# Kernel optimization log

Measured on AMD Instinct MI355X. Metric: run time of the kernel, lower is better.

Reference implementation:

```python
import jax, jax.numpy as jnp
import numpy as np

N = 100000      # nodes
E = 3200000     # edges (avg degree 32)
D = 128         # in_channels
H = 128         # hidden_channels
L = 4           # num_layers
G = 1000        # graphs in batch
C = 10          # out_channels
BN_EPS = 1e-5


def _init(key, shape, fan_in):
    return jax.random.normal(key, shape, jnp.float32) * jnp.float32(1.0 / np.sqrt(fan_in))


def setup_inputs() -> dict:
    key = jax.random.key(0)
    ks = jax.random.split(key, 12)
    x = jax.random.normal(ks[0], (N, D), jnp.float32)
    edge_index = jax.random.randint(ks[1], (2, E), 0, N)
    batch = jnp.sort(jax.random.randint(ks[2], (N,), 0, G))
    # stacked per-layer GINConv MLP params (in==hidden so all layers share shapes)
    W1 = _init(ks[3], (L, D, 2 * H), D)
    b1 = jnp.zeros((L, 2 * H), jnp.float32)
    g1 = jnp.ones((L, 2 * H), jnp.float32)
    bt1 = jnp.zeros((L, 2 * H), jnp.float32)
    W2 = _init(ks[4], (L, 2 * H, H), 2 * H)
    b2 = jnp.zeros((L, H), jnp.float32)
    g2 = jnp.ones((L, H), jnp.float32)
    bt2 = jnp.zeros((L, H), jnp.float32)
    eps = jnp.zeros((L,), jnp.float32)  # train_eps=True, init 0
    # final graph-level MLP
    Wm1 = _init(ks[5], (H, H), H)
    bm1 = jnp.zeros((H,), jnp.float32)
    gm = jnp.ones((H,), jnp.float32)
    btm = jnp.zeros((H,), jnp.float32)
    Wm2 = _init(ks[6], (H, C), H)
    bm2 = jnp.zeros((C,), jnp.float32)
    return dict(x=x, edge_index=edge_index, batch=batch, eps=eps,
                W1=W1, b1=b1, g1=g1, bt1=bt1, W2=W2, b2=b2, g2=g2, bt2=bt2,
                Wm1=Wm1, bm1=bm1, gm=gm, btm=btm, Wm2=Wm2, bm2=bm2)


def batchnorm(z, g, b):
    # training-mode BN: batch statistics, biased variance (torch semantics)
    m = jnp.mean(z, axis=0)
    v = jnp.mean(jnp.square(z - m), axis=0)
    return (z - m) * (g * jax.lax.rsqrt(v + BN_EPS)) + b


def reference(x, edge_index, batch, eps, W1, b1, g1, bt1, W2, b2, g2, bt2,
              Wm1, bm1, gm, btm, Wm2, bm2):
    src, dst = edge_index[0], edge_index[1]
    h = x
    for l in range(L):
        # GINConv: (1+eps)*x_i + sum_{j in N(i)} x_j, then MLP
        agg = jax.ops.segment_sum(h[src], dst, num_segments=N)  # [N, d]
        z = (1.0 + eps[l]) * h + agg
        z = jax.nn.relu(batchnorm(z @ W1[l] + b1[l], g1[l], bt1[l]))
        h = z @ W2[l] + b2[l]
        # outer per-layer BatchNorm + relu
        h = jax.nn.relu(batchnorm(h, g2[l], bt2[l]))
    # global_add_pool over graphs
    ge = jax.ops.segment_sum(h, batch, num_segments=G)  # [G, H]
    o = jax.nn.relu(batchnorm(ge @ Wm1 + bm1, gm, btm))  # dropout = identity (eval)
    return o @ Wm2 + bm2  # [G, C]
```

## Files before the change

kernel.cpp:

```cpp
#include <hip/hip_runtime.h>

#define N_NODES 100000
#define N_EDGES 3200000
#define NGRAPH  1000
#define NOUT    10
#define BN_EPS  1e-5f
#define CAP     96

#define SUM1 0
#define SQ1  256
#define S1   512
#define SH1  768
#define SUM2 1024
#define SQ2  1152
#define S2   1280
#define SH2  1408
#define SUMG 1536
#define SQG  1664
#define SG   1792
#define SHG  1920

typedef short v8s __attribute__((ext_vector_type(8)));
typedef float v4f __attribute__((ext_vector_type(4)));

__device__ __forceinline__ unsigned short f2bf(float x) {
    unsigned u = __float_as_uint(x);
    u += 0x7FFFu + ((u >> 16) & 1u);
    return (unsigned short)(u >> 16);
}
__device__ __forceinline__ float bf2f(unsigned short h) {
    return __uint_as_float(((unsigned)h) << 16);
}


__global__ void k_zero_i(int* p, int n) {
    int i = blockIdx.x * 256 + threadIdx.x;
    if (i < n) p[i] = 0;
}

__global__ void k_fillb(const int* __restrict__ ei, int* __restrict__ cnt,
                        int* __restrict__ csr) {
    const int lo = blockIdx.x * 12500;
    const int base = blockIdx.y * 2048 + threadIdx.x;
#pragma unroll
    for (int i = 0; i < 8; ++i) {
        int e = base + i * 256;
        if (e < N_EDGES) {
            int d = ei[N_EDGES + e];
            if ((unsigned)(d - lo) < 12500u) {
                int slot = atomicAdd(&cnt[d], 1);
                if (slot < CAP) csr[d * CAP + slot] = ei[e];
            }
        }
    }
}


__global__ void k_cvt0(const float* __restrict__ x, unsigned short* __restrict__ hb) {
    int i = blockIdx.x * 256 + threadIdx.x;
    float4 v = ((const float4*)x)[i];
    ushort4 o;
    o.x = f2bf(v.x); o.y = f2bf(v.y); o.z = f2bf(v.z); o.w = f2bf(v.w);
    ((ushort4*)hb)[i] = o;
}


__global__ void k_bnapply(const unsigned short* __restrict__ hb,
                          unsigned short* __restrict__ yb,
                          const float* __restrict__ s, const float* __restrict__ sh) {
    int i = blockIdx.x * 256 + threadIdx.x;
    int c16 = i & 15;
    uint4 u = ((const uint4*)hb)[i];
    float4 sA = ((const float4*)s)[c16 * 2], sB = ((const float4*)s)[c16 * 2 + 1];
    float4 hA = ((const float4*)sh)[c16 * 2], hB = ((const float4*)sh)[c16 * 2 + 1];
    float y0 = fmaxf(fmaf(__uint_as_float(u.x << 16),        sA.x, hA.x), 0.f);
    float y1 = fmaxf(fmaf(__uint_as_float(u.x & 0xffff0000u), sA.y, hA.y), 0.f);
    float y2 = fmaxf(fmaf(__uint_as_float(u.y << 16),        sA.z, hA.z), 0.f);
    float y3 = fmaxf(fmaf(__uint_as_float(u.y & 0xffff0000u), sA.w, hA.w), 0.f);
    float y4 = fmaxf(fmaf(__uint_as_float(u.z << 16),        sB.x, hB.x), 0.f);
    float y5 = fmaxf(fmaf(__uint_as_float(u.z & 0xffff0000u), sB.y, hB.y), 0.f);
    float y6 = fmaxf(fmaf(__uint_as_float(u.w << 16),        sB.z, hB.z), 0.f);
    float y7 = fmaxf(fmaf(__uint_as_float(u.w & 0xffff0000u), sB.w, hB.w), 0.f);
    uint4 o;
    o.x = (unsigned)f2bf(y0) | ((unsigned)f2bf(y1) << 16);
    o.y = (unsigned)f2bf(y2) | ((unsigned)f2bf(y3) << 16);
    o.z = (unsigned)f2bf(y4) | ((unsigned)f2bf(y5) << 16);
    o.w = (unsigned)f2bf(y6) | ((unsigned)f2bf(y7) << 16);
    ((uint4*)yb)[i] = o;
}


__global__ void k_wsplit(const float* __restrict__ W1l, const float* __restrict__ W2l,
                         unsigned short* __restrict__ w1h, unsigned short* __restrict__ w1lo,
                         unsigned short* __restrict__ w2h, unsigned short* __restrict__ w2lo) {
    int idx = blockIdx.x * 256 + threadIdx.x;
    if (idx < 32768) {
        float v = W1l[idx];
        int k = idx >> 8, n = idx & 255;
        unsigned short h = f2bf(v);
        unsigned short l = f2bf(v - bf2f(h));
        int o = n * 128 + k;
        w1h[o] = h; w1lo[o] = l;
    } else {
        int i2 = idx - 32768;
        float v = W2l[i2];
        int k = i2 >> 7, n = i2 & 127;
        unsigned short h = f2bf(v);
        unsigned short l = f2bf(v - bf2f(h));
        int o = n * 256 + k;
        w2h[o] = h; w2lo[o] = l;
    }
}


__launch_bounds__(256)
__global__ void k_agg(const unsigned short* __restrict__ yb, unsigned short* __restrict__ zh,
                      unsigned short* __restrict__ zl, const int* __restrict__ cnt,
                      const int* __restrict__ csr, const float* __restrict__ eps, int l,
                      float* __restrict__ stats) {
    if (blockIdx.x == 0) {
        int t = threadIdx.x;
        stats[SUM1 + t] = 0.f;
        stats[SQ1 + t] = 0.f;
        if (t < 128) { stats[SUM2 + t] = 0.f; stats[SQ2 + t] = 0.f; }
    }
    const int tid = threadIdx.x;
    const int wid = tid >> 6, lane = tid & 63;
    const int q = lane >> 4, sl = lane & 15;
    const int node = blockIdx.x * 16 + wid * 4 + q;
    const uint4* y4 = (const uint4*)yb;
    const size_t selfo = (size_t)node * 16 + sl;

    float epv = 1.f + eps[l];
    uint4 su = y4[selfo];
    float acc[8];
    acc[0] = epv * __uint_as_float(su.x << 16);
    acc[1] = epv * __uint_as_float(su.x & 0xffff0000u);
    acc[2] = epv * __uint_as_float(su.y << 16);
    acc[3] = epv * __uint_as_float(su.y & 0xffff0000u);
    acc[4] = epv * __uint_as_float(su.z << 16);
    acc[5] = epv * __uint_as_float(su.z & 0xffff0000u);
    acc[6] = epv * __uint_as_float(su.w << 16);
    acc[7] = epv * __uint_as_float(su.w & 0xffff0000u);

    int d = min(cnt[node], CAP);
    const int* row = csr + node * CAP;
    int t = 0;
    for (; t + 3 < d; t += 4) {
        int4 jv = *(const int4*)(row + t);
        uint4 v0 = y4[(size_t)jv.x * 16 + sl];
        uint4 v1 = y4[(size_t)jv.y * 16 + sl];
        uint4 v2 = y4[(size_t)jv.z * 16 + sl];
        uint4 v3 = y4[(size_t)jv.w * 16 + sl];
        acc[0] += __uint_as_float(v0.x << 16);
        acc[1] += __uint_as_float(v0.x & 0xffff0000u);
        acc[2] += __uint_as_float(v0.y << 16);
        acc[3] += __uint_as_float(v0.y & 0xffff0000u);
        acc[4] += __uint_as_float(v0.z << 16);
        acc[5] += __uint_as_float(v0.z & 0xffff0000u);
        acc[6] += __uint_as_float(v0.w << 16);
        acc[7] += __uint_as_float(v0.w & 0xffff0000u);
        acc[0] += __uint_as_float(v1.x << 16);
        acc[1] += __uint_as_float(v1.x & 0xffff0000u);
        acc[2] += __uint_as_float(v1.y << 16);
        acc[3] += __uint_as_float(v1.y & 0xffff0000u);
        acc[4] += __uint_as_float(v1.z << 16);
        acc[5] += __uint_as_float(v1.z & 0xffff0000u);
        acc[6] += __uint_as_float(v1.w << 16);
        acc[7] += __uint_as_float(v1.w & 0xffff0000u);
        acc[0] += __uint_as_float(v2.x << 16);
        acc[1] += __uint_as_float(v2.x & 0xffff0000u);
        acc[2] += __uint_as_float(v2.y << 16);
        acc[3] += __uint_as_float(v2.y & 0xffff0000u);
        acc[4] += __uint_as_float(v2.z << 16);
        acc[5] += __uint_as_float(v2.z & 0xffff0000u);
        acc[6] += __uint_as_float(v2.w << 16);
        acc[7] += __uint_as_float(v2.w & 0xffff0000u);
        acc[0] += __uint_as_float(v3.x << 16);
        acc[1] += __uint_as_float(v3.x & 0xffff0000u);
        acc[2] += __uint_as_float(v3.y << 16);
        acc[3] += __uint_as_float(v3.y & 0xffff0000u);
        acc[4] += __uint_as_float(v3.z << 16);
        acc[5] += __uint_as_float(v3.z & 0xffff0000u);
        acc[6] += __uint_as_float(v3.w << 16);
        acc[7] += __uint_as_float(v3.w & 0xffff0000u);
    }
    for (; t < d; ++t) {
        uint4 v = y4[(size_t)row[t] * 16 + sl];
        acc[0] += __uint_as_float(v.x << 16);
        acc[1] += __uint_as_float(v.x & 0xffff0000u);
        acc[2] += __uint_as_float(v.y << 16);
        acc[3] += __uint_as_float(v.y & 0xffff0000u);
        acc[4] += __uint_as_float(v.z << 16);
        acc[5] += __uint_as_float(v.z & 0xffff0000u);
        acc[6] += __uint_as_float(v.w << 16);
        acc[7] += __uint_as_float(v.w & 0xffff0000u);
    }

    unsigned oh[4], ol[4];
#pragma unroll
    for (int w = 0; w < 4; ++w) {
        float a = acc[2 * w], b = acc[2 * w + 1];
        unsigned short ha = f2bf(a), hb_ = f2bf(b);
        unsigned short la = f2bf(a - bf2f(ha)), lb = f2bf(b - bf2f(hb_));
        oh[w] = (unsigned)ha | ((unsigned)hb_ << 16);
        ol[w] = (unsigned)la | ((unsigned)lb << 16);
    }
    uint4 vh; vh.x = oh[0]; vh.y = oh[1]; vh.z = oh[2]; vh.w = oh[3];
    uint4 vl; vl.x = ol[0]; vl.y = ol[1]; vl.z = ol[2]; vl.w = ol[3];
    ((uint4*)zh)[selfo] = vh;
    ((uint4*)zl)[selfo] = vl;
}


template <int K, int NC>
__launch_bounds__(256, 2)
__global__ void k_mgemm1(const unsigned short* __restrict__ Azh,
                         const unsigned short* __restrict__ Azl,
                         const unsigned short* __restrict__ Bhi,
                         const unsigned short* __restrict__ Blo,
                         const float* __restrict__ bias, float* __restrict__ Cm, int M,
                         float* __restrict__ osum, float* __restrict__ osq) {
    __shared__ unsigned short Ash[128 * 72];
    __shared__ unsigned short Asl[128 * 72];
    __shared__ unsigned short Bsh[128 * 72];
    __shared__ unsigned short Bsl[128 * 72];
    const int tid = threadIdx.x;
    const int lane = tid & 63;
    const int wid = tid >> 6;
    const int wm = wid >> 1, wn = wid & 1;
    const int lr = lane & 15;
    const int q = lane >> 4;
    const int r0 = blockIdx.x * 128;
    const int c0 = blockIdx.y * 128;

    v4f acc[16];
#pragma unroll
    for (int i = 0; i < 16; ++i) acc[i] = (v4f){0.f, 0.f, 0.f, 0.f};

    for (int kc = 0; kc < K; kc += 64) {
#pragma unroll
        for (int it = 0; it < 4; ++it) {
            int li = it * 256 + tid;
            int row = li >> 3, s8 = li & 7;
            int r = r0 + row;
            float4 vh = make_float4(0.f, 0.f, 0.f, 0.f);
            float4 vl = vh;
            if (r < M) {
                size_t go = (size_t)r * K + kc + s8 * 8;
                vh = *(const float4*)(Azh + go);
                vl = *(const float4*)(Azl + go);
            }
            int off = row * 72 + s8 * 8;
            *(float4*)&Ash[off] = vh;
            *(float4*)&Asl[off] = vl;
        }
#pragma unroll
        for (int it = 0; it < 4; ++it) {
            int li = it * 256 + tid;
            int n = li >> 3, s8 = li & 7;
            int off = n * 72 + s8 * 8;
            size_t go = (size_t)(c0 + n) * K + kc + s8 * 8;
            *(float4*)&Bsh[off] = *(const float4*)(Bhi + go);
            *(float4*)&Bsl[off] = *(const float4*)(Blo + go);
        }
        __syncthreads();
#pragma unroll
        for (int kk = 0; kk < 2; ++kk) {
            v8s ah[4], al[4], bh[4], bl[4];
#pragma unroll
            for (int t = 0; t < 4; ++t) {
                int aoff = (wm * 64 + t * 16 + lr) * 72 + kk * 32 + q * 8;
                ah[t] = *(const v8s*)&Ash[aoff];
                al[t] = *(const v8s*)&Asl[aoff];
                int boff = (wn * 64 + t * 16 + lr) * 72 + kk * 32 + q * 8;
                bh[t] = *(const v8s*)&Bsh[boff];
                bl[t] = *(const v8s*)&Bsl[boff];
            }
#pragma unroll
            for (int mt = 0; mt < 4; ++mt)
#pragma unroll
                for (int nt = 0; nt < 4; ++nt)
                    acc[mt * 4 + nt] = __builtin_amdgcn_mfma_f32_16x16x32_bf16(
                        ah[mt], bh[nt], acc[mt * 4 + nt], 0, 0, 0);
#pragma unroll
            for (int mt = 0; mt < 4; ++mt)
#pragma unroll
                for (int nt = 0; nt < 4; ++nt)
                    acc[mt * 4 + nt] = __builtin_amdgcn_mfma_f32_16x16x32_bf16(
                        ah[mt], bl[nt], acc[mt * 4 + nt], 0, 0, 0);
#pragma unroll
            for (int mt = 0; mt < 4; ++mt)
#pragma unroll
                for (int nt = 0; nt < 4; ++nt)
                    acc[mt * 4 + nt] = __builtin_amdgcn_mfma_f32_16x16x32_bf16(
                        al[mt], bh[nt], acc[mt * 4 + nt], 0, 0, 0);
        }
        __syncthreads();
    }

    float bias_v[4];
#pragma unroll
    for (int nt = 0; nt < 4; ++nt) bias_v[nt] = bias[c0 + wn * 64 + nt * 16 + lr];
    float ps[4] = {0.f, 0.f, 0.f, 0.f}, pq[4] = {0.f, 0.f, 0.f, 0.f};
#pragma unroll
    for (int mt = 0; mt < 4; ++mt) {
        int rb = r0 + wm * 64 + mt * 16 + q * 4;
#pragma unroll
        for (int r = 0; r < 4; ++r) {
            int row = rb + r;
            if (row < M) {
#pragma unroll
                for (int nt = 0; nt < 4; ++nt) {
                    float o = acc[mt * 4 + nt][r] + bias_v[nt];
                    Cm[(size_t)row * NC + c0 + wn * 64 + nt * 16 + lr] = o;
                    ps[nt] += o;
                    pq[nt] += o * o;
                }
            }
        }
    }
#pragma unroll
    for (int nt = 0; nt < 4; ++nt) {
        ps[nt] += __shfl_down(ps[nt], 16);
        ps[nt] += __shfl_down(ps[nt], 32);
        pq[nt] += __shfl_down(pq[nt], 16);
        pq[nt] += __shfl_down(pq[nt], 32);
    }
    if (lane < 16) {
#pragma unroll
        for (int nt = 0; nt < 4; ++nt) {
            int col = c0 + wn * 64 + nt * 16 + lane;
            atomicAdd(&osum[col], ps[nt]);
            atomicAdd(&osq[col], pq[nt]);
        }
    }
}


template <int K, int NC>
__launch_bounds__(256, 2)
__global__ void k_mgemm2(const float* __restrict__ A, const unsigned short* __restrict__ Bhi,
                         const unsigned short* __restrict__ Blo, const float* __restrict__ bias,
                         unsigned short* __restrict__ Cb, int M,
                         const float* __restrict__ ain_s, const float* __restrict__ ain_sh,
                         float* __restrict__ osum, float* __restrict__ osq) {
    __shared__ unsigned short Ash[128 * 72];
    __shared__ unsigned short Asl[128 * 72];
    __shared__ unsigned short Bsh[128 * 72];
    __shared__ unsigned short Bsl[128 * 72];
    const int tid = threadIdx.x;
    const int lane = tid & 63;
    const int wid = tid >> 6;
    const int wm = wid >> 1, wn = wid & 1;
    const int lr = lane & 15;
    const int q = lane >> 4;
    const int r0 = blockIdx.x * 128;
    const int c0 = blockIdx.y * 128;

    v4f acc[16];
#pragma unroll
    for (int i = 0; i < 16; ++i) acc[i] = (v4f){0.f, 0.f, 0.f, 0.f};

    for (int kc = 0; kc < K; kc += 64) {
#pragma unroll
        for (int it = 0; it < 8; ++it) {
            int li = it * 256 + tid;
            int row = li >> 4, s4 = li & 15;
            int r = r0 + row;
            float4 v = make_float4(0.f, 0.f, 0.f, 0.f);
            if (r < M) {
                v = *(const float4*)(A + (size_t)r * K + kc + s4 * 4);
                float4 s = *(const float4*)(ain_s + kc + s4 * 4);
                float4 h = *(const float4*)(ain_sh + kc + s4 * 4);
                v.x = fmaxf(fmaf(v.x, s.x, h.x), 0.f);
                v.y = fmaxf(fmaf(v.y, s.y, h.y), 0.f);
                v.z = fmaxf(fmaf(v.z, s.z, h.z), 0.f);
                v.w = fmaxf(fmaf(v.w, s.w, h.w), 0.f);
            }
            unsigned short h0 = f2bf(v.x), h1 = f2bf(v.y), h2 = f2bf(v.z), h3 = f2bf(v.w);
            unsigned short l0 = f2bf(v.x - bf2f(h0)), l1 = f2bf(v.y - bf2f(h1));
            unsigned short l2 = f2bf(v.z - bf2f(h2)), l3 = f2bf(v.w - bf2f(h3));
            int off = row * 72 + s4 * 4;
            *(short4*)&Ash[off] = make_short4((short)h0, (short)h1, (short)h2, (short)h3);
            *(short4*)&Asl[off] = make_short4((short)l0, (short)l1, (short)l2, (short)l3);
        }
#pragma unroll
        for (int it = 0; it < 4; ++it) {
            int li = it * 256 + tid;
            int n = li >> 3, s8 = li & 7;
            int off = n * 72 + s8 * 8;
            size_t go = (size_t)(c0 + n) * K + kc + s8 * 8;
            *(float4*)&Bsh[off] = *(const float4*)(Bhi + go);
            *(float4*)&Bsl[off] = *(const float4*)(Blo + go);
        }
        __syncthreads();
#pragma unroll
        for (int kk = 0; kk < 2; ++kk) {
            v8s ah[4], al[4], bh[4], bl[4];
#pragma unroll
            for (int t = 0; t < 4; ++t) {
                int aoff = (wm * 64 + t * 16 + lr) * 72 + kk * 32 + q * 8;
                ah[t] = *(const v8s*)&Ash[aoff];
                al[t] = *(const v8s*)&Asl[aoff];
                int boff = (wn * 64 + t * 16 + lr) * 72 + kk * 32 + q * 8;
                bh[t] = *(const v8s*)&Bsh[boff];
                bl[t] = *(const v8s*)&Bsl[boff];
            }
#pragma unroll
            for (int mt = 0; mt < 4; ++mt)
#pragma unroll
                for (int nt = 0; nt < 4; ++nt)
                    acc[mt * 4 + nt] = __builtin_amdgcn_mfma_f32_16x16x32_bf16(
                        ah[mt], bh[nt], acc[mt * 4 + nt], 0, 0, 0);
#pragma unroll
            for (int mt = 0; mt < 4; ++mt)
#pragma unroll
                for (int nt = 0; nt < 4; ++nt)
                    acc[mt * 4 + nt] = __builtin_amdgcn_mfma_f32_16x16x32_bf16(
                        ah[mt], bl[nt], acc[mt * 4 + nt], 0, 0, 0);
#pragma unroll
            for (int mt = 0; mt < 4; ++mt)
#pragma unroll
                for (int nt = 0; nt < 4; ++nt)
                    acc[mt * 4 + nt] = __builtin_amdgcn_mfma_f32_16x16x32_bf16(
                        al[mt], bh[nt], acc[mt * 4 + nt], 0, 0, 0);
        }
        __syncthreads();
    }

    float bias_v[4];
#pragma unroll
    for (int nt = 0; nt < 4; ++nt) bias_v[nt] = bias[c0 + wn * 64 + nt * 16 + lr];
    float ps[4] = {0.f, 0.f, 0.f, 0.f}, pq[4] = {0.f, 0.f, 0.f, 0.f};
#pragma unroll
    for (int mt = 0; mt < 4; ++mt) {
        int rb = r0 + wm * 64 + mt * 16 + q * 4;
#pragma unroll
        for (int r = 0; r < 4; ++r) {
            int row = rb + r;
            if (row < M) {
#pragma unroll
                for (int nt = 0; nt < 4; ++nt) {
                    float o = acc[mt * 4 + nt][r] + bias_v[nt];
                    Cb[(size_t)row * NC + c0 + wn * 64 + nt * 16 + lr] = f2bf(o);
                    ps[nt] += o;
                    pq[nt] += o * o;
                }
            }
        }
    }
#pragma unroll
    for (int nt = 0; nt < 4; ++nt) {
        ps[nt] += __shfl_down(ps[nt], 16);
        ps[nt] += __shfl_down(ps[nt], 32);
        pq[nt] += __shfl_down(pq[nt], 16);
        pq[nt] += __shfl_down(pq[nt], 32);
    }
    if (lane < 16) {
#pragma unroll
        for (int nt = 0; nt < 4; ++nt) {
            int col = c0 + wn * 64 + nt * 16 + lane;
            atomicAdd(&osum[col], ps[nt]);
            atomicAdd(&osq[col], pq[nt]);
        }
    }
}


template <int K, int NC, bool AIN, bool STATS>
__launch_bounds__(256)
__global__ void k_gemm(const float* __restrict__ A, const float* __restrict__ Bg,
                       const float* __restrict__ bias, float* __restrict__ Cm, int M,
                       const float* __restrict__ ain_s, const float* __restrict__ ain_sh,
                       float* __restrict__ osum, float* __restrict__ osq) {
    __shared__ __align__(16) float As[64][68];
    __shared__ __align__(16) float Bs[64][68];
    const int tid = threadIdx.x;
    const int tx = tid & 15, ty = tid >> 4;
    const int r0 = blockIdx.x * 64;
    const int c0 = blockIdx.y * 64;
    float acc[4][4] = {};

    for (int kc = 0; kc < K; kc += 64) {
#pragma unroll
        for (int it = 0; it < 4; ++it) {
            int li = it * 256 + tid;
            int row = li >> 4, f4 = li & 15;
            int r = r0 + row;
            float4 v = make_float4(0.f, 0.f, 0.f, 0.f);
            if (r < M) v = *(const float4*)(A + (size_t)r * K + kc + f4 * 4);
            As[f4 * 4 + 0][row] = v.x;
            As[f4 * 4 + 1][row] = v.y;
            As[f4 * 4 + 2][row] = v.z;
            As[f4 * 4 + 3][row] = v.w;
        }
#pragma unroll
        for (int it = 0; it < 4; ++it) {
            int li = it * 256 + tid;
            int krow = li >> 4, f4 = li & 15;
            float4 v = *(const float4*)(Bg + (size_t)(kc + krow) * NC + c0 + f4 * 4);
            *(float4*)&Bs[krow][f4 * 4] = v;
        }
        __syncthreads();
#pragma unroll
        for (int k = 0; k < 64; ++k) {
            float4 a = *(const float4*)&As[k][ty * 4];
            float4 b = *(const float4*)&Bs[k][tx * 4];
            float av[4] = {a.x, a.y, a.z, a.w};
            float bv[4] = {b.x, b.y, b.z, b.w};
#pragma unroll
            for (int i = 0; i < 4; ++i)
#pragma unroll
                for (int j = 0; j < 4; ++j) acc[i][j] = fmaf(av[i], bv[j], acc[i][j]);
        }
        __syncthreads();
    }

    const int c = c0 + tx * 4;
    float4 bb = *(const float4*)(bias + c);
    float bvv[4] = {bb.x, bb.y, bb.z, bb.w};
    float ps[4] = {0.f, 0.f, 0.f, 0.f};
    float pq[4] = {0.f, 0.f, 0.f, 0.f};
#pragma unroll
    for (int i = 0; i < 4; ++i) {
        int r = r0 + ty * 4 + i;
        if (r < M) {
            float o[4];
#pragma unroll
            for (int j = 0; j < 4; ++j) {
                o[j] = acc[i][j] + bvv[j];
                if (STATS) { ps[j] += o[j]; pq[j] += o[j] * o[j]; }
            }
            float4 ov = make_float4(o[0], o[1], o[2], o[3]);
            *(float4*)(Cm + (size_t)r * NC + c) = ov;
        }
    }
    if (STATS) {
        float* rs = &As[0][0];
        float* rq = &Bs[0][0];
        *(float4*)&rs[ty * 68 + tx * 4] = make_float4(ps[0], ps[1], ps[2], ps[3]);
        *(float4*)&rq[ty * 68 + tx * 4] = make_float4(pq[0], pq[1], pq[2], pq[3]);
        __syncthreads();
        if (tid < 16) {
#pragma unroll
            for (int j = 0; j < 4; ++j) {
                float s = 0.f, q = 0.f;
                for (int t = 0; t < 16; ++t) {
                    s += rs[t * 68 + tid * 4 + j];
                    q += rq[t * 68 + tid * 4 + j];
                }
                atomicAdd(&osum[c0 + tid * 4 + j], s);
                atomicAdd(&osq[c0 + tid * 4 + j], q);
            }
        }
    }
}


__global__ void k_bnstats(const float* __restrict__ sum, const float* __restrict__ sq,
                          const float* __restrict__ g, const float* __restrict__ bt,
                          float* __restrict__ s, float* __restrict__ sh, int n, float invM) {
    int i = threadIdx.x;
    if (i < n) {
        float m = sum[i] * invM;
        float v = sq[i] * invM - m * m;
        float sc = g[i] * rsqrtf(v + BN_EPS);
        s[i] = sc;
        sh[i] = bt[i] - m * sc;
    }
}


__global__ void k_zero2_f(float* p1, int n1, float* p2, int n2) {
    int i = blockIdx.x * 256 + threadIdx.x;
    if (i < n1) p1[i] = 0.f;
    else if (i - n1 < n2) p2[i - n1] = 0.f;
}

__global__ void k_pool(const unsigned short* __restrict__ hb, const int* __restrict__ batch,
                       float* __restrict__ ge, const float* __restrict__ s,
                       const float* __restrict__ sh) {
    int t = blockIdx.x * 256 + threadIdx.x;
    int c = t & 63;
    int n0 = (t >> 6) * 8;
    float2 sv = ((const float2*)s)[c];
    float2 shv = ((const float2*)sh)[c];
    const unsigned* h2 = (const unsigned*)hb;
    float ax = 0.f, ay = 0.f;
    int gcur = batch[n0];
#pragma unroll
    for (int k = 0; k < 8; ++k) {
        int n = n0 + k;
        int g = batch[n];
        if (g != gcur) {
            float* p = ge + (size_t)gcur * 128 + c * 2;
            atomicAdd(p, ax);
            atomicAdd(p + 1, ay);
            ax = 0.f; ay = 0.f; gcur = g;
        }
        unsigned u = h2[(size_t)n * 64 + c];
        ax += fmaxf(fmaf(__uint_as_float(u << 16), sv.x, shv.x), 0.f);
        ay += fmaxf(fmaf(__uint_as_float(u & 0xffff0000u), sv.y, shv.y), 0.f);
    }
    float* p = ge + (size_t)gcur * 128 + c * 2;
    atomicAdd(p, ax);
    atomicAdd(p + 1, ay);
}


__global__ void k_final(const float* __restrict__ gmid, const float* __restrict__ sg,
                        const float* __restrict__ shg, const float* __restrict__ Wm2,
                        const float* __restrict__ bm2, float* __restrict__ out) {
    int idx = blockIdx.x * 256 + threadIdx.x;
    if (idx >= NGRAPH * NOUT) return;
    int g = idx / NOUT, c = idx % NOUT;
    const float* row = gmid + (size_t)g * 128;
    float acc = bm2[c];
#pragma unroll 8
    for (int k = 0; k < 128; ++k) {
        float y = fmaxf(fmaf(row[k], sg[k], shg[k]), 0.f);
        acc = fmaf(y, Wm2[k * NOUT + c], acc);
    }
    out[idx] = acc;
}


extern "C" void kernel_launch(void* const* d_in, const int* in_sizes, int n_in,
                              void* d_out, int out_size, void* d_ws, size_t ws_size,
                              hipStream_t stream) {
    const float* x   = (const float*)d_in[0];
    const int*   ei  = (const int*)d_in[1];
    const int* batch = (const int*)d_in[2];
    const float* eps = (const float*)d_in[3];
    const float* W1  = (const float*)d_in[4];
    const float* b1  = (const float*)d_in[5];
    const float* g1  = (const float*)d_in[6];
    const float* bt1 = (const float*)d_in[7];
    const float* W2  = (const float*)d_in[8];
    const float* b2  = (const float*)d_in[9];
    const float* g2  = (const float*)d_in[10];
    const float* bt2 = (const float*)d_in[11];
    const float* Wm1 = (const float*)d_in[12];
    const float* bm1 = (const float*)d_in[13];
    const float* gm  = (const float*)d_in[14];
    const float* btm = (const float*)d_in[15];
    const float* Wm2 = (const float*)d_in[16];
    const float* bm2 = (const float*)d_in[17];
    float* out = (float*)d_out;

    float* W = (float*)d_ws;
    float* bufC  = W;
    float* stats = W + 25600000;
    float* ge    = W + 25602048;
    float* gmid  = W + 25730048;
    int* ib      = (int*)(W + 25858048);
    int* cnt = ib;
    int* csr = ib + 100000;
    unsigned short* wt = (unsigned short*)(ib + 9700000);
    unsigned short* w1h = wt;
    unsigned short* w1l = wt + 32768;
    unsigned short* w2h = wt + 65536;
    unsigned short* w2l = wt + 98304;
    unsigned short* hb = wt + 131072;
    unsigned short* zh = hb + 12800000;
    unsigned short* zl = zh + 12800000;
    unsigned short* yb = zl + 12800000;

    k_zero_i<<<391, 256, 0, stream>>>(cnt, N_NODES);
    k_fillb<<<dim3(8, 1563), 256, 0, stream>>>(ei, cnt, csr);
    k_cvt0<<<12500, 256, 0, stream>>>(x, hb);

    for (int l = 0; l < 4; ++l) {
        k_wsplit<<<256, 256, 0, stream>>>(W1 + l * 32768, W2 + l * 32768,
                                          w1h, w1l, w2h, w2l);
        const unsigned short* ysrc;
        if (l == 0) {
            ysrc = hb;
        } else {
            k_bnapply<<<6250, 256, 0, stream>>>(hb, yb, stats + S2, stats + SH2);
            ysrc = yb;
        }
        k_agg<<<6250, 256, 0, stream>>>(ysrc, zh, zl, cnt, csr, eps, l, stats);
        k_mgemm1<128, 256><<<dim3(782, 2), 256, 0, stream>>>(
            zh, zl, w1h, w1l, b1 + l * 256, bufC, N_NODES, stats + SUM1, stats + SQ1);
        k_bnstats<<<1, 256, 0, stream>>>(stats + SUM1, stats + SQ1, g1 + l * 256,
                                         bt1 + l * 256, stats + S1, stats + SH1, 256,
                                         1.f / N_NODES);
        k_mgemm2<256, 128><<<dim3(782, 1), 256, 0, stream>>>(
            bufC, w2h, w2l, b2 + l * 128, hb, N_NODES,
            stats + S1, stats + SH1, stats + SUM2, stats + SQ2);
        k_bnstats<<<1, 128, 0, stream>>>(stats + SUM2, stats + SQ2, g2 + l * 128,
                                         bt2 + l * 128, stats + S2, stats + SH2, 128,
                                         1.f / N_NODES);
    }

    k_zero2_f<<<502, 256, 0, stream>>>(ge, 128000, stats + SUMG, 256);
    k_pool<<<3125, 256, 0, stream>>>(hb, batch, ge, stats + S2, stats + SH2);
    k_gemm<128, 128, false, true><<<dim3(16, 2), 256, 0, stream>>>(
        ge, Wm1, bm1, gmid, NGRAPH, nullptr, nullptr, stats + SUMG, stats + SQG);
    k_bnstats<<<1, 128, 0, stream>>>(stats + SUMG, stats + SQG, gm, btm,
                                     stats + SG, stats + SHG, 128, 1.f / NGRAPH);
    k_final<<<40, 256, 0, stream>>>(gmid, stats + SG, stats + SHG, Wm2, bm2, out);
}
```

Measured before the change: 1.513 ms.

## Use direct global-to-LDS loads with XOR swizzle in GEMMs, truncating split, finer CSR build

The GEMM kernels now stage tiles through global_load_lds (direct global-to-LDS DMA) into an unpadded, XOR-swizzled LDS layout instead of going through registers into a padded layout. This cuts VGPR traffic and LDS use per block. The hi/lo bf16 split now truncates instead of rounding, which saves ALU work but slightly changes the precision split. The CSR fill kernel uses 32 destination partitions instead of 8, which lowers atomic contention at the cost of reading the edge list more often. One risk is that the A-tile loads in mgemm1 no longer guard rows past M on the last tile, so they may read out of bounds.

```diff
diff --git a/kernel.cpp b/kernel.cpp
--- a/kernel.cpp
+++ b/kernel.cpp
@@ -1,4 +1,5 @@
 #include <hip/hip_runtime.h>
+#include <stdint.h>
 
 #define N_NODES 100000
 #define N_EDGES 3200000
@@ -32,6 +33,20 @@
     return __uint_as_float(((unsigned)h) << 16);
 }
 
+__device__ __forceinline__ void gl_lds16(const void* g, void* l) {
+    __builtin_amdgcn_global_load_lds(
+        (const __attribute__((address_space(1))) unsigned int*)g,
+        (__attribute__((address_space(3))) unsigned int*)l, 16, 0, 0);
+}
+
+__device__ __forceinline__ void split2(float a, float b, unsigned& hi, unsigned& lo) {
+    unsigned ua = __float_as_uint(a), ub = __float_as_uint(b);
+    hi = (ua >> 16) | (ub & 0xffff0000u);
+    float ra = a - __uint_as_float(ua & 0xffff0000u);
+    float rb = b - __uint_as_float(ub & 0xffff0000u);
+    lo = (__float_as_uint(ra) >> 16) | (__float_as_uint(rb) & 0xffff0000u);
+}
+
 
 __global__ void k_zero_i(int* p, int n) {
     int i = blockIdx.x * 256 + threadIdx.x;
@@ -40,14 +55,14 @@
 
 __global__ void k_fillb(const int* __restrict__ ei, int* __restrict__ cnt,
                         int* __restrict__ csr) {
-    const int lo = blockIdx.x * 12500;
+    const int lo = (blockIdx.z * 8 + blockIdx.x) * 3125;
     const int base = blockIdx.y * 2048 + threadIdx.x;
 #pragma unroll
     for (int i = 0; i < 8; ++i) {
         int e = base + i * 256;
         if (e < N_EDGES) {
             int d = ei[N_EDGES + e];
-            if ((unsigned)(d - lo) < 12500u) {
+            if ((unsigned)(d - lo) < 3125u) {
                 int slot = atomicAdd(&cnt[d], 1);
                 if (slot < CAP) csr[d * CAP + slot] = ei[e];
             }
@@ -197,17 +212,11 @@
         acc[7] += __uint_as_float(v.w & 0xffff0000u);
     }
 
-    unsigned oh[4], ol[4];
-#pragma unroll
-    for (int w = 0; w < 4; ++w) {
-        float a = acc[2 * w], b = acc[2 * w + 1];
-        unsigned short ha = f2bf(a), hb_ = f2bf(b);
-        unsigned short la = f2bf(a - bf2f(ha)), lb = f2bf(b - bf2f(hb_));
-        oh[w] = (unsigned)ha | ((unsigned)hb_ << 16);
-        ol[w] = (unsigned)la | ((unsigned)lb << 16);
-    }
-    uint4 vh; vh.x = oh[0]; vh.y = oh[1]; vh.z = oh[2]; vh.w = oh[3];
-    uint4 vl; vl.x = ol[0]; vl.y = ol[1]; vl.z = ol[2]; vl.w = ol[3];
+    uint4 vh, vl;
+    split2(acc[0], acc[1], vh.x, vl.x);
+    split2(acc[2], acc[3], vh.y, vl.y);
+    split2(acc[4], acc[5], vh.z, vl.z);
+    split2(acc[6], acc[7], vh.w, vl.w);
     ((uint4*)zh)[selfo] = vh;
     ((uint4*)zl)[selfo] = vl;
 }
@@ -221,16 +230,17 @@
                          const unsigned short* __restrict__ Blo,
                          const float* __restrict__ bias, float* __restrict__ Cm, int M,
                          float* __restrict__ osum, float* __restrict__ osq) {
-    __shared__ unsigned short Ash[128 * 72];
-    __shared__ unsigned short Asl[128 * 72];
-    __shared__ unsigned short Bsh[128 * 72];
-    __shared__ unsigned short Bsl[128 * 72];
+    __shared__ unsigned short Ash[128 * 64];
+    __shared__ unsigned short Asl[128 * 64];
+    __shared__ unsigned short Bsh[128 * 64];
+    __shared__ unsigned short Bsl[128 * 64];
     const int tid = threadIdx.x;
     const int lane = tid & 63;
     const int wid = tid >> 6;
     const int wm = wid >> 1, wn = wid & 1;
     const int lr = lane & 15;
     const int q = lane >> 4;
+    const int e7 = lr & 7;
     const int r0 = blockIdx.x * 128;
     const int c0 = blockIdx.y * 128;
 
@@ -239,43 +249,33 @@
     for (int i = 0; i < 16; ++i) acc[i] = (v4f){0.f, 0.f, 0.f, 0.f};
 
     for (int kc = 0; kc < K; kc += 64) {
-#pragma unroll
-        for (int it = 0; it < 4; ++it) {
-            int li = it * 256 + tid;
-            int row = li >> 3, s8 = li & 7;
-            int r = r0 + row;
-            float4 vh = make_float4(0.f, 0.f, 0.f, 0.f);
-            float4 vl = vh;
-            if (r < M) {
-                size_t go = (size_t)r * K + kc + s8 * 8;
-                vh = *(const float4*)(Azh + go);
-                vl = *(const float4*)(Azl + go);
-            }
-            int off = row * 72 + s8 * 8;
-            *(float4*)&Ash[off] = vh;
-            *(float4*)&Asl[off] = vl;
-        }
-#pragma unroll
-        for (int it = 0; it < 4; ++it) {
-            int li = it * 256 + tid;
-            int n = li >> 3, s8 = li & 7;
-            int off = n * 72 + s8 * 8;
-            size_t go = (size_t)(c0 + n) * K + kc + s8 * 8;
-            *(float4*)&Bsh[off] = *(const float4*)(Bhi + go);
-            *(float4*)&Bsl[off] = *(const float4*)(Blo + go);
+        const int sb = wid * 256;
+#pragma unroll
+        for (int j = 0; j < 4; ++j) {
+            int slot = sb + j * 64 + lane;
+            int row = slot >> 3, sl = slot & 7;
+            int sg = sl ^ (row & 7);
+            size_t ga = (size_t)(r0 + row) * K + kc + sg * 8;
+            size_t gb = (size_t)(c0 + row) * K + kc + sg * 8;
+            int lb = (sb + j * 64) * 8;
+            gl_lds16(Azh + ga, &Ash[lb]);
+            gl_lds16(Azl + ga, &Asl[lb]);
+            gl_lds16(Bhi + gb, &Bsh[lb]);
+            gl_lds16(Blo + gb, &Bsl[lb]);
         }
         __syncthreads();
 #pragma unroll
         for (int kk = 0; kk < 2; ++kk) {
+            const int sg = (((kk << 2) + q) ^ e7) * 8;
             v8s ah[4], al[4], bh[4], bl[4];
 #pragma unroll
             for (int t = 0; t < 4; ++t) {
-                int aoff = (wm * 64 + t * 16 + lr) * 72 + kk * 32 + q * 8;
-                ah[t] = *(const v8s*)&Ash[aoff];
-                al[t] = *(const v8s*)&Asl[aoff];
-                int boff = (wn * 64 + t * 16 + lr) * 72 + kk * 32 + q * 8;
-                bh[t] = *(const v8s*)&Bsh[boff];
-                bl[t] = *(const v8s*)&Bsl[boff];
+                int ar = (wm * 64 + t * 16 + lr) * 64 + sg;
+                ah[t] = *(const v8s*)&Ash[ar];
+                al[t] = *(const v8s*)&Asl[ar];
+                int br = (wn * 64 + t * 16 + lr) * 64 + sg;
+                bh[t] = *(const v8s*)&Bsh[br];
+                bl[t] = *(const v8s*)&Bsl[br];
             }
 #pragma unroll
             for (int mt = 0; mt < 4; ++mt)
@@ -345,16 +345,17 @@
                          unsigned short* __restrict__ Cb, int M,
                          const float* __restrict__ ain_s, const float* __restrict__ ain_sh,
                          float* __restrict__ osum, float* __restrict__ osq) {
-    __shared__ unsigned short Ash[128 * 72];
-    __shared__ unsigned short Asl[128 * 72];
-    __shared__ unsigned short Bsh[128 * 72];
-    __shared__ unsigned short Bsl[128 * 72];
+    __shared__ unsigned short Ash[128 * 64];
+    __shared__ unsigned short Asl[128 * 64];
+    __shared__ unsigned short Bsh[128 * 64];
+    __shared__ unsigned short Bsl[128 * 64];
     const int tid = threadIdx.x;
     const int lane = tid & 63;
     const int wid = tid >> 6;
     const int wm = wid >> 1, wn = wid & 1;
     const int lr = lane & 15;
     const int q = lane >> 4;
+    const int e7 = lr & 7;
     const int r0 = blockIdx.x * 128;
     const int c0 = blockIdx.y * 128;
 
@@ -363,6 +364,17 @@
     for (int i = 0; i < 16; ++i) acc[i] = (v4f){0.f, 0.f, 0.f, 0.f};
 
     for (int kc = 0; kc < K; kc += 64) {
+        const int sb = wid * 256;
+#pragma unroll
+        for (int j = 0; j < 4; ++j) {
+            int slot = sb + j * 64 + lane;
+            int row = slot >> 3, sl = slot & 7;
+            int sg = sl ^ (row & 7);
+            size_t gb = (size_t)(c0 + row) * K + kc + sg * 8;
+            int lb = (sb + j * 64) * 8;
+            gl_lds16(Bhi + gb, &Bsh[lb]);
+            gl_lds16(Blo + gb, &Bsl[lb]);
+        }
 #pragma unroll
         for (int it = 0; it < 8; ++it) {
             int li = it * 256 + tid;
@@ -378,34 +390,26 @@
                 v.z = fmaxf(fmaf(v.z, s.z, h.z), 0.f);
                 v.w = fmaxf(fmaf(v.w, s.w, h.w), 0.f);
             }
-            unsigned short h0 = f2bf(v.x), h1 = f2bf(v.y), h2 = f2bf(v.z), h3 = f2bf(v.w);
-            unsigned short l0 = f2bf(v.x - bf2f(h0)), l1 = f2bf(v.y - bf2f(h1));
-            unsigned short l2 = f2bf(v.z - bf2f(h2)), l3 = f2bf(v.w - bf2f(h3));
-            int off = row * 72 + s4 * 4;
-            *(short4*)&Ash[off] = make_short4((short)h0, (short)h1, (short)h2, (short)h3);
-            *(short4*)&Asl[off] = make_short4((short)l0, (short)l1, (short)l2, (short)l3);
-        }
-#pragma unroll
-        for (int it = 0; it < 4; ++it) {
-            int li = it * 256 + tid;
-            int n = li >> 3, s8 = li & 7;
-            int off = n * 72 + s8 * 8;
-            size_t go = (size_t)(c0 + n) * K + kc + s8 * 8;
-            *(float4*)&Bsh[off] = *(const float4*)(Bhi + go);
-            *(float4*)&Bsl[off] = *(const float4*)(Blo + go);
+            uint2 hp, lp;
+            split2(v.x, v.y, hp.x, lp.x);
+            split2(v.z, v.w, hp.y, lp.y);
+            int ou = row * 32 + (((s4 >> 1) ^ (row & 7)) << 2) + ((s4 & 1) << 1);
+            *(uint2*)&((unsigned*)Ash)[ou] = hp;
+            *(uint2*)&((unsigned*)Asl)[ou] = lp;
         }
         __syncthreads();
 #pragma unroll
         for (int kk = 0; kk < 2; ++kk) {
+            const int sg = (((kk << 2) + q) ^ e7) * 8;
             v8s ah[4], al[4], bh[4], bl[4];
 #pragma unroll
             for (int t = 0; t < 4; ++t) {
-                int aoff = (wm * 64 + t * 16 + lr) * 72 + kk * 32 + q * 8;
-                ah[t] = *(const v8s*)&Ash[aoff];
-                al[t] = *(const v8s*)&Asl[aoff];
-                int boff = (wn * 64 + t * 16 + lr) * 72 + kk * 32 + q * 8;
-                bh[t] = *(const v8s*)&Bsh[boff];
-                bl[t] = *(const v8s*)&Bsl[boff];
+                int ar = (wm * 64 + t * 16 + lr) * 64 + sg;
+                ah[t] = *(const v8s*)&Ash[ar];
+                al[t] = *(const v8s*)&Asl[ar];
+                int br = (wn * 64 + t * 16 + lr) * 64 + sg;
+                bh[t] = *(const v8s*)&Bsh[br];
+                bl[t] = *(const v8s*)&Bsl[br];
             }
 #pragma unroll
             for (int mt = 0; mt < 4; ++mt)
@@ -668,7 +672,7 @@
     unsigned short* yb = zl + 12800000;
 
     k_zero_i<<<391, 256, 0, stream>>>(cnt, N_NODES);
-    k_fillb<<<dim3(8, 1563), 256, 0, stream>>>(ei, cnt, csr);
+    k_fillb<<<dim3(8, 1563, 4), 256, 0, stream>>>(ei, cnt, csr);
     k_cvt0<<<12500, 256, 0, stream>>>(x, hb);
 
     for (int l = 0; l < 4; ++l) {
```

After: 1.582 ms. +4.6%, slower.
